# Optimization experiments

Measured on AMD Instinct MI355X. Metric: run time of the kernel, lower is better.

The kernel has to match this reference:

```python
import jax, jax.numpy as jnp
import numpy as np

FACTORS = (32, 32, 32)  # prod = 32768 feature dim
BATCH = 2048


def setup_inputs() -> dict:
    key = jax.random.key(0)
    k0, k1, k2, k3 = jax.random.split(key, 4)
    N = int(np.prod(FACTORS))
    x = jax.random.normal(k0, (BATCH, N), dtype=jnp.float32)
    # scale weights ~1/sqrt(f) so outputs stay O(1) through 3 contractions
    s = 1.0 / np.sqrt(FACTORS[0])
    W1 = jax.random.normal(k1, (FACTORS[0], FACTORS[0]), dtype=jnp.float32) * s
    W2 = jax.random.normal(k2, (FACTORS[1], FACTORS[1]), dtype=jnp.float32) * s
    W3 = jax.random.normal(k3, (FACTORS[2], FACTORS[2]), dtype=jnp.float32) * s
    return {"x": x, "W1": W1, "W2": W2, "W3": W3}


def reference(x, W1, W2, W3):
    # Factorized (Kronecker) linear: y = x with each factor axis contracted
    # against its factor matrix (x.view(-1, f) @ W_f per factor, axes cycled).
    B = x.shape[0]
    f1, f2, f3 = FACTORS
    x = x.reshape(B, f1, f2, f3)
    x = jnp.einsum('bpqr,pi->biqr', x, W1)  # contract factor-1 axis
    x = jnp.einsum('biqr,qj->bijr', x, W2)  # contract factor-2 axis
    x = jnp.einsum('bijr,rk->bijk', x, W3)  # contract factor-3 axis
    return x.reshape(B, f1 * f2 * f3)
```

## Files before the change

### kernel.cpp

```cpp
#include <hip/hip_runtime.h>
#include <hip/hip_bf16.h>


typedef __attribute__((ext_vector_type(8))) short bf16x8;
typedef __attribute__((ext_vector_type(4))) float f32x4;

#define NROW 32768

__device__ __forceinline__ unsigned short f2b(float f) {
    union { float f; unsigned u; } v; v.f = f;
    unsigned r = v.u + 0x7fffu + ((v.u >> 16) & 1u);
    return (unsigned short)(r >> 16);
}

__device__ __forceinline__ int swz(int row, int col) {
    int s = ((row ^ (row >> 2) ^ (row >> 4)) & 3) << 3;
    return row * 32 + (col ^ s);
}

__device__ __forceinline__ bf16x8 wfrag(const float* __restrict__ W, int h, int c, int g) {
    bf16x8 r;
#pragma unroll
    for (int j = 0; j < 8; ++j)
        r[j] = (short)f2b(W[(8 * g + j) * 32 + 16 * h + c]);
    return r;
}

__device__ __forceinline__ bf16x8 ldsfrag(const unsigned short* buf, int row, int g) {
    int s = (row ^ (row >> 2) ^ (row >> 4)) & 3;
    union { uint4 u; bf16x8 b; } cv;
    cv.u = *(const uint4*)(buf + row * 32 + 8 * (g ^ s));
    return cv.b;
}

__global__ __launch_bounds__(1024, 8) void kron3_mfma(
    const float* __restrict__ x,  const float* __restrict__ W1,
    const float* __restrict__ W2, const float* __restrict__ W3,
    float* __restrict__ out)
{
    __shared__ unsigned short buf[NROW];
    const int t = threadIdx.x;
    const int w = t >> 6, c = t & 15, g = (t >> 4) & 3;
    const float* __restrict__ xrow = x + (size_t)blockIdx.x * NROW;
    float* __restrict__ orow = out + (size_t)blockIdx.x * NROW;
    const f32x4 vzero = {0.f, 0.f, 0.f, 0.f};

    bf16x8 fa[4];
#pragma unroll
    for (int mt = 0; mt < 4; ++mt) {
        const float* src = xrow + (64 * w + 16 * mt + c) * 32 + 8 * g;
        float4 f0 = ((const float4*)src)[0];
        float4 f1 = ((const float4*)src)[1];
        bf16x8 r;
        r[0] = (short)f2b(f0.x); r[1] = (short)f2b(f0.y);
        r[2] = (short)f2b(f0.z); r[3] = (short)f2b(f0.w);
        r[4] = (short)f2b(f1.x); r[5] = (short)f2b(f1.y);
        r[6] = (short)f2b(f1.z); r[7] = (short)f2b(f1.w);
        fa[mt] = r;
    }
    bf16x8 wA[2];
    wA[0] = wfrag(W3, 0, c, g);
    wA[1] = wfrag(W3, 1, c, g);

#pragma unroll
    for (int nt = 0; nt < 2; ++nt) {
        const int kp = 16 * nt + c;
#pragma unroll
        for (int mt = 0; mt < 4; ++mt) {
            f32x4 a = __builtin_amdgcn_mfma_f32_16x16x32_bf16(fa[mt], wA[nt], vzero, 0, 0, 0);
            const int p  = 2 * w + (mt >> 1);
            const int q0 = 16 * (mt & 1) + 4 * g;
            unsigned lo = (unsigned)f2b(a[0]) | ((unsigned)f2b(a[1]) << 16);
            unsigned hi = (unsigned)f2b(a[2]) | ((unsigned)f2b(a[3]) << 16);
            *(uint2*)(buf + swz(p * 32 + kp, q0)) = make_uint2(lo, hi);
        }
    }

    bf16x8 fb[4];
#pragma unroll
    for (int mt = 0; mt < 4; ++mt)
        fb[mt] = ldsfrag(buf, 64 * w + 16 * mt + c, g);
    bf16x8 wB[2];
    wB[0] = wfrag(W2, 0, c, g);
    wB[1] = wfrag(W2, 1, c, g);
    __syncthreads();

#pragma unroll
    for (int jt = 0; jt < 2; ++jt) {
#pragma unroll
        for (int mt = 0; mt < 4; ++mt) {
            f32x4 a = __builtin_amdgcn_mfma_f32_16x16x32_bf16(wB[jt], fb[mt], vzero, 0, 0, 0);
            const int k = 16 * (mt & 1) + c;
            const int p = 2 * w + (mt >> 1);
#pragma unroll
            for (int rg = 0; rg < 4; ++rg) {
                const int j = 16 * jt + 4 * g + rg;
                buf[swz(j * 32 + k, p)] = f2b(a[rg]);
            }
        }
    }
    __syncthreads();

    bf16x8 wC[2];
    wC[0] = wfrag(W1, 0, c, g);
    wC[1] = wfrag(W1, 1, c, g);
    bf16x8 fc[4];
#pragma unroll
    for (int mt = 0; mt < 4; ++mt)
        fc[mt] = ldsfrag(buf, 64 * w + 16 * mt + c, g);

#pragma unroll
    for (int nt = 0; nt < 2; ++nt) {
        const int i = 16 * nt + c;
#pragma unroll
        for (int mt = 0; mt < 4; ++mt) {
            f32x4 a = __builtin_amdgcn_mfma_f32_16x16x32_bf16(fc[mt], wC[nt], vzero, 0, 0, 0);
            const int j  = 2 * w + (mt >> 1);
            const int k0 = 16 * (mt & 1) + 4 * g;
            *(float4*)(orow + i * 1024 + j * 32 + k0) =
                make_float4(a[0], a[1], a[2], a[3]);
        }
    }
}

extern "C" void kernel_launch(void* const* d_in, const int* in_sizes, int n_in,
                              void* d_out, int out_size, void* d_ws, size_t ws_size,
                              hipStream_t stream) {
    const float* x  = (const float*)d_in[0];
    const float* W1 = (const float*)d_in[1];
    const float* W2 = (const float*)d_in[2];
    const float* W3 = (const float*)d_in[3];
    float* outp = (float*)d_out;

    const int batch = in_sizes[0] / NROW;
    kron3_mfma<<<dim3(batch), dim3(1024), 0, stream>>>(x, W1, W2, W3, outp);
}
```

Measured before the change: 122.7 us.

## Make kernel persistent over batch rows with register prefetch of next row

Launches a fixed grid of 512 blocks of 512 threads, each looping over batch rows (4 per block) and doing twice the work per thread. The next row's x data is loaded into registers during the current row's stage-2 work, so global loads overlap compute. Also switches bf16 conversion to packed intrinsics and uses lighter custom barriers. In exchange it raises register pressure and reduces the number of blocks, which could limit latency hiding. It also assumes the batch divides evenly by 512.

New measurement: 428.5 us. +249.1%, slower.

```diff
diff --git a/kernel.cpp b/kernel.cpp
--- a/kernel.cpp
+++ b/kernel.cpp
@@ -6,11 +6,29 @@
 typedef __attribute__((ext_vector_type(4))) float f32x4;
 
 #define NROW 32768
+#define NBLK 512
 
-__device__ __forceinline__ unsigned short f2b(float f) {
-    union { float f; unsigned u; } v; v.f = f;
-    unsigned r = v.u + 0x7fffu + ((v.u >> 16) & 1u);
-    return (unsigned short)(r >> 16);
+#define BAR() do {                                          \
+    asm volatile("s_waitcnt lgkmcnt(0)" ::: "memory");      \
+    __builtin_amdgcn_s_barrier();                           \
+    __builtin_amdgcn_sched_barrier(0);                      \
+} while (0)
+
+__device__ __forceinline__ unsigned pk2(float a, float b) {
+    union { __hip_bfloat162 h; unsigned u; } v;
+    v.h = __float22bfloat162_rn(make_float2(a, b));
+    return v.u;
+}
+__device__ __forceinline__ unsigned short b16(float a) {
+    union { __hip_bfloat16 h; unsigned short u; } v;
+    v.h = __float2bfloat16(a);
+    return v.u;
+}
+__device__ __forceinline__ bf16x8 packfrag(float4 f0, float4 f1) {
+    union { unsigned u[4]; bf16x8 b; } r;
+    r.u[0] = pk2(f0.x, f0.y); r.u[1] = pk2(f0.z, f0.w);
+    r.u[2] = pk2(f1.x, f1.y); r.u[3] = pk2(f1.z, f1.w);
+    return r.b;
 }
 
 __device__ __forceinline__ int swz(int row, int col) {
@@ -19,11 +37,14 @@
 }
 
 __device__ __forceinline__ bf16x8 wfrag(const float* __restrict__ W, int h, int c, int g) {
-    bf16x8 r;
+    union { unsigned u[4]; bf16x8 b; } r;
 #pragma unroll
-    for (int j = 0; j < 8; ++j)
-        r[j] = (short)f2b(W[(8 * g + j) * 32 + 16 * h + c]);
-    return r;
+    for (int jj = 0; jj < 4; ++jj) {
+        float a = W[(8 * g + 2 * jj    ) * 32 + 16 * h + c];
+        float b = W[(8 * g + 2 * jj + 1) * 32 + 16 * h + c];
+        r.u[jj] = pk2(a, b);
+    }
+    return r.b;
 }
 
 __device__ __forceinline__ bf16x8 ldsfrag(const unsigned short* buf, int row, int g) {
@@ -33,92 +54,110 @@
     return cv.b;
 }
 
-__global__ __launch_bounds__(1024, 8) void kron3_mfma(
+__global__ __launch_bounds__(512, 4) void kron3_mfma(
     const float* __restrict__ x,  const float* __restrict__ W1,
     const float* __restrict__ W2, const float* __restrict__ W3,
-    float* __restrict__ out)
+    float* __restrict__ out, int iters)
 {
     __shared__ unsigned short buf[NROW];
     const int t = threadIdx.x;
     const int w = t >> 6, c = t & 15, g = (t >> 4) & 3;
-    const float* __restrict__ xrow = x + (size_t)blockIdx.x * NROW;
-    float* __restrict__ orow = out + (size_t)blockIdx.x * NROW;
     const f32x4 vzero = {0.f, 0.f, 0.f, 0.f};
 
-    bf16x8 fa[4];
+    float4 fr[16];
+    {
+        const float* xr = x + (size_t)blockIdx.x * NROW;
 #pragma unroll
-    for (int mt = 0; mt < 4; ++mt) {
-        const float* src = xrow + (64 * w + 16 * mt + c) * 32 + 8 * g;
-        float4 f0 = ((const float4*)src)[0];
-        float4 f1 = ((const float4*)src)[1];
-        bf16x8 r;
-        r[0] = (short)f2b(f0.x); r[1] = (short)f2b(f0.y);
-        r[2] = (short)f2b(f0.z); r[3] = (short)f2b(f0.w);
-        r[4] = (short)f2b(f1.x); r[5] = (short)f2b(f1.y);
-        r[6] = (short)f2b(f1.z); r[7] = (short)f2b(f1.w);
-        fa[mt] = r;
-    }
-    bf16x8 wA[2];
-    wA[0] = wfrag(W3, 0, c, g);
-    wA[1] = wfrag(W3, 1, c, g);
-
-#pragma unroll
-    for (int nt = 0; nt < 2; ++nt) {
-        const int kp = 16 * nt + c;
-#pragma unroll
-        for (int mt = 0; mt < 4; ++mt) {
-            f32x4 a = __builtin_amdgcn_mfma_f32_16x16x32_bf16(fa[mt], wA[nt], vzero, 0, 0, 0);
-            const int p  = 2 * w + (mt >> 1);
-            const int q0 = 16 * (mt & 1) + 4 * g;
-            unsigned lo = (unsigned)f2b(a[0]) | ((unsigned)f2b(a[1]) << 16);
-            unsigned hi = (unsigned)f2b(a[2]) | ((unsigned)f2b(a[3]) << 16);
-            *(uint2*)(buf + swz(p * 32 + kp, q0)) = make_uint2(lo, hi);
+        for (int mt = 0; mt < 8; ++mt) {
+            const float* s = xr + (128 * w + 16 * mt + c) * 32 + 8 * g;
+            fr[2 * mt]     = ((const float4*)s)[0];
+            fr[2 * mt + 1] = ((const float4*)s)[1];
         }
     }
+    bf16x8 fa[8];
+#pragma unroll
+    for (int mt = 0; mt < 8; ++mt) fa[mt] = packfrag(fr[2 * mt], fr[2 * mt + 1]);
 
-    bf16x8 fb[4];
+#pragma unroll 1
+    for (int it = 0; it < iters; ++it) {
+        int tv = t;
+        asm volatile("" : "+v"(tv));
+        const int cv = tv & 15, gv = (tv >> 4) & 3;
+
+        {
+            bf16x8 wA[2] = { wfrag(W3, 0, cv, gv), wfrag(W3, 1, cv, gv) };
 #pragma unroll
-    for (int mt = 0; mt < 4; ++mt)
-        fb[mt] = ldsfrag(buf, 64 * w + 16 * mt + c, g);
-    bf16x8 wB[2];
-    wB[0] = wfrag(W2, 0, c, g);
-    wB[1] = wfrag(W2, 1, c, g);
-    __syncthreads();
-
+            for (int nt = 0; nt < 2; ++nt) {
+                const int kp = 16 * nt + c;
 #pragma unroll
-    for (int jt = 0; jt < 2; ++jt) {
-#pragma unroll
-        for (int mt = 0; mt < 4; ++mt) {
-            f32x4 a = __builtin_amdgcn_mfma_f32_16x16x32_bf16(wB[jt], fb[mt], vzero, 0, 0, 0);
-            const int k = 16 * (mt & 1) + c;
-            const int p = 2 * w + (mt >> 1);
-#pragma unroll
-            for (int rg = 0; rg < 4; ++rg) {
-                const int j = 16 * jt + 4 * g + rg;
-                buf[swz(j * 32 + k, p)] = f2b(a[rg]);
+                for (int mt = 0; mt < 8; ++mt) {
+                    f32x4 a = __builtin_amdgcn_mfma_f32_16x16x32_bf16(fa[mt], wA[nt], vzero, 0, 0, 0);
+                    const int p  = 4 * w + (mt >> 1);
+                    const int q0 = 16 * (mt & 1) + 4 * g;
+                    *(uint2*)(buf + swz(p * 32 + kp, q0)) =
+                        make_uint2(pk2(a[0], a[1]), pk2(a[2], a[3]));
+                }
             }
         }
-    }
-    __syncthreads();
 
-    bf16x8 wC[2];
-    wC[0] = wfrag(W1, 0, c, g);
-    wC[1] = wfrag(W1, 1, c, g);
-    bf16x8 fc[4];
+        bf16x8 fb[8];
 #pragma unroll
-    for (int mt = 0; mt < 4; ++mt)
-        fc[mt] = ldsfrag(buf, 64 * w + 16 * mt + c, g);
+        for (int mt = 0; mt < 8; ++mt)
+            fb[mt] = ldsfrag(buf, 128 * w + 16 * mt + c, g);
 
+        if (it + 1 < iters) {
+            const float* xr = x + (size_t)(blockIdx.x + NBLK * (it + 1)) * NROW;
 #pragma unroll
-    for (int nt = 0; nt < 2; ++nt) {
-        const int i = 16 * nt + c;
+            for (int mt = 0; mt < 8; ++mt) {
+                const float* s = xr + (128 * w + 16 * mt + c) * 32 + 8 * g;
+                fr[2 * mt]     = ((const float4*)s)[0];
+                fr[2 * mt + 1] = ((const float4*)s)[1];
+            }
+        }
+        BAR();
+
+        {
+            bf16x8 wB[2] = { wfrag(W2, 0, cv, gv), wfrag(W2, 1, cv, gv) };
 #pragma unroll
-        for (int mt = 0; mt < 4; ++mt) {
-            f32x4 a = __builtin_amdgcn_mfma_f32_16x16x32_bf16(fc[mt], wC[nt], vzero, 0, 0, 0);
-            const int j  = 2 * w + (mt >> 1);
-            const int k0 = 16 * (mt & 1) + 4 * g;
-            *(float4*)(orow + i * 1024 + j * 32 + k0) =
-                make_float4(a[0], a[1], a[2], a[3]);
+            for (int jt = 0; jt < 2; ++jt) {
+#pragma unroll
+                for (int mt = 0; mt < 8; ++mt) {
+                    f32x4 a = __builtin_amdgcn_mfma_f32_16x16x32_bf16(wB[jt], fb[mt], vzero, 0, 0, 0);
+                    const int k = 16 * (mt & 1) + c;
+                    const int p = 4 * w + (mt >> 1);
+#pragma unroll
+                    for (int rg = 0; rg < 4; ++rg)
+                        buf[swz((16 * jt + 4 * g + rg) * 32 + k, p)] = b16(a[rg]);
+                }
+            }
+        }
+        if (it + 1 < iters) {
+#pragma unroll
+            for (int mt = 0; mt < 8; ++mt) fa[mt] = packfrag(fr[2 * mt], fr[2 * mt + 1]);
+        }
+        BAR();
+
+        bf16x8 fc[8];
+#pragma unroll
+        for (int mt = 0; mt < 8; ++mt)
+            fc[mt] = ldsfrag(buf, 128 * w + 16 * mt + c, g);
+        BAR();
+
+        {
+            bf16x8 wC[2] = { wfrag(W1, 0, cv, gv), wfrag(W1, 1, cv, gv) };
+            float* orow = out + (size_t)(blockIdx.x + NBLK * it) * NROW;
+#pragma unroll
+            for (int nt = 0; nt < 2; ++nt) {
+                const int i = 16 * nt + c;
+#pragma unroll
+                for (int mt = 0; mt < 8; ++mt) {
+                    f32x4 a = __builtin_amdgcn_mfma_f32_16x16x32_bf16(fc[mt], wC[nt], vzero, 0, 0, 0);
+                    const int j  = 4 * w + (mt >> 1);
+                    const int k0 = 16 * (mt & 1) + 4 * g;
+                    *(float4*)(orow + i * 1024 + j * 32 + k0) =
+                        make_float4(a[0], a[1], a[2], a[3]);
+                }
+            }
         }
     }
 }
@@ -133,5 +172,6 @@
     float* outp = (float*)d_out;
 
     const int batch = in_sizes[0] / NROW;
-    kron3_mfma<<<dim3(batch), dim3(1024), 0, stream>>>(x, W1, W2, W3, outp);
+    const int iters = batch / NBLK;
+    kron3_mfma<<<dim3(NBLK), dim3(512), 0, stream>>>(x, W1, W2, W3, outp, iters);
 }
```

## Vectorize LDS writes via transposed intermediate layout, hardware bf16 packing, nontemporal stores

Applied to the files above, without the earlier changes.

Reorders the shared-memory intermediate layout so the second contraction computes x·W2 and writes packed 64-bit bf16 pairs instead of scalar 16-bit stores. It also replaces the manual round-to-nearest bf16 conversion with the packed float2-to-bfloat162 intrinsic, and makes the final output stores nontemporal. The new layout spreads each wave's writes across rows owned by other waves, so an extra block barrier is added after the first stage. The aim is to cut LDS store instructions and conversion ALU work, and to reduce cache pollution from the streaming output.

After: 121.2 us. About the same (-1.3%).

```diff
diff --git a/kernel.cpp b/kernel.cpp
--- a/kernel.cpp
+++ b/kernel.cpp
@@ -7,10 +7,16 @@
 
 #define NROW 32768
 
-__device__ __forceinline__ unsigned short f2b(float f) {
-    union { float f; unsigned u; } v; v.f = f;
-    unsigned r = v.u + 0x7fffu + ((v.u >> 16) & 1u);
-    return (unsigned short)(r >> 16);
+__device__ __forceinline__ unsigned pk2(float a, float b) {
+    union { __hip_bfloat162 h; unsigned u; } v;
+    v.h = __float22bfloat162_rn(make_float2(a, b));
+    return v.u;
+}
+__device__ __forceinline__ bf16x8 packfrag(float4 f0, float4 f1) {
+    union { unsigned u[4]; bf16x8 b; } r;
+    r.u[0] = pk2(f0.x, f0.y); r.u[1] = pk2(f0.z, f0.w);
+    r.u[2] = pk2(f1.x, f1.y); r.u[3] = pk2(f1.z, f1.w);
+    return r.b;
 }
 
 __device__ __forceinline__ int swz(int row, int col) {
@@ -19,11 +25,14 @@
 }
 
 __device__ __forceinline__ bf16x8 wfrag(const float* __restrict__ W, int h, int c, int g) {
-    bf16x8 r;
+    union { unsigned u[4]; bf16x8 b; } r;
 #pragma unroll
-    for (int j = 0; j < 8; ++j)
-        r[j] = (short)f2b(W[(8 * g + j) * 32 + 16 * h + c]);
-    return r;
+    for (int jj = 0; jj < 4; ++jj) {
+        float a = W[(8 * g + 2 * jj    ) * 32 + 16 * h + c];
+        float b = W[(8 * g + 2 * jj + 1) * 32 + 16 * h + c];
+        r.u[jj] = pk2(a, b);
+    }
+    return r.b;
 }
 
 __device__ __forceinline__ bf16x8 ldsfrag(const unsigned short* buf, int row, int g) {
@@ -48,19 +57,12 @@
     bf16x8 fa[4];
 #pragma unroll
     for (int mt = 0; mt < 4; ++mt) {
-        const float* src = xrow + (64 * w + 16 * mt + c) * 32 + 8 * g;
-        float4 f0 = ((const float4*)src)[0];
-        float4 f1 = ((const float4*)src)[1];
-        bf16x8 r;
-        r[0] = (short)f2b(f0.x); r[1] = (short)f2b(f0.y);
-        r[2] = (short)f2b(f0.z); r[3] = (short)f2b(f0.w);
-        r[4] = (short)f2b(f1.x); r[5] = (short)f2b(f1.y);
-        r[6] = (short)f2b(f1.z); r[7] = (short)f2b(f1.w);
-        fa[mt] = r;
+        const float* s = xrow + (64 * w + 16 * mt + c) * 32 + 8 * g;
+        float4 f0 = ((const float4*)s)[0];
+        float4 f1 = ((const float4*)s)[1];
+        fa[mt] = packfrag(f0, f1);
     }
-    bf16x8 wA[2];
-    wA[0] = wfrag(W3, 0, c, g);
-    wA[1] = wfrag(W3, 1, c, g);
+    bf16x8 wA[2] = { wfrag(W3, 0, c, g), wfrag(W3, 1, c, g) };
 
 #pragma unroll
     for (int nt = 0; nt < 2; ++nt) {
@@ -70,44 +72,38 @@
             f32x4 a = __builtin_amdgcn_mfma_f32_16x16x32_bf16(fa[mt], wA[nt], vzero, 0, 0, 0);
             const int p  = 2 * w + (mt >> 1);
             const int q0 = 16 * (mt & 1) + 4 * g;
-            unsigned lo = (unsigned)f2b(a[0]) | ((unsigned)f2b(a[1]) << 16);
-            unsigned hi = (unsigned)f2b(a[2]) | ((unsigned)f2b(a[3]) << 16);
-            *(uint2*)(buf + swz(p * 32 + kp, q0)) = make_uint2(lo, hi);
+            *(uint2*)(buf + swz(kp * 32 + p, q0)) =
+                make_uint2(pk2(a[0], a[1]), pk2(a[2], a[3]));
         }
     }
+    __syncthreads();
 
     bf16x8 fb[4];
 #pragma unroll
     for (int mt = 0; mt < 4; ++mt)
         fb[mt] = ldsfrag(buf, 64 * w + 16 * mt + c, g);
-    bf16x8 wB[2];
-    wB[0] = wfrag(W2, 0, c, g);
-    wB[1] = wfrag(W2, 1, c, g);
+    bf16x8 wB[2] = { wfrag(W2, 0, c, g), wfrag(W2, 1, c, g) };
     __syncthreads();
 
 #pragma unroll
-    for (int jt = 0; jt < 2; ++jt) {
+    for (int nt = 0; nt < 2; ++nt) {
+        const int j = 16 * nt + c;
 #pragma unroll
         for (int mt = 0; mt < 4; ++mt) {
-            f32x4 a = __builtin_amdgcn_mfma_f32_16x16x32_bf16(wB[jt], fb[mt], vzero, 0, 0, 0);
-            const int k = 16 * (mt & 1) + c;
-            const int p = 2 * w + (mt >> 1);
-#pragma unroll
-            for (int rg = 0; rg < 4; ++rg) {
-                const int j = 16 * jt + 4 * g + rg;
-                buf[swz(j * 32 + k, p)] = f2b(a[rg]);
-            }
+            f32x4 a = __builtin_amdgcn_mfma_f32_16x16x32_bf16(fb[mt], wB[nt], vzero, 0, 0, 0);
+            const int kq = 2 * w + (mt >> 1);
+            const int p0 = 16 * (mt & 1) + 4 * g;
+            *(uint2*)(buf + swz(j * 32 + kq, p0)) =
+                make_uint2(pk2(a[0], a[1]), pk2(a[2], a[3]));
         }
     }
     __syncthreads();
 
-    bf16x8 wC[2];
-    wC[0] = wfrag(W1, 0, c, g);
-    wC[1] = wfrag(W1, 1, c, g);
     bf16x8 fc[4];
 #pragma unroll
     for (int mt = 0; mt < 4; ++mt)
         fc[mt] = ldsfrag(buf, 64 * w + 16 * mt + c, g);
+    bf16x8 wC[2] = { wfrag(W1, 0, c, g), wfrag(W1, 1, c, g) };
 
 #pragma unroll
     for (int nt = 0; nt < 2; ++nt) {
@@ -117,8 +113,8 @@
             f32x4 a = __builtin_amdgcn_mfma_f32_16x16x32_bf16(fc[mt], wC[nt], vzero, 0, 0, 0);
             const int j  = 2 * w + (mt >> 1);
             const int k0 = 16 * (mt & 1) + 4 * g;
-            *(float4*)(orow + i * 1024 + j * 32 + k0) =
-                make_float4(a[0], a[1], a[2], a[3]);
+            __builtin_nontemporal_store(a,
+                (f32x4*)(orow + i * 1024 + j * 32 + k0));
         }
     }
 }
```
